# Performance work log

Hardware: AMD Instinct MI355X
Metric: run time of the kernel (lower is better)

Reference implementation:

```python
import jax, jax.numpy as jnp
import numpy as np
from jax import lax

EPS = 1e-5
PH = PW = 2  # patch size

def _bn(x, g, b, m, v):
    # eval-mode BatchNorm2d on NCHW
    scale = (g / jnp.sqrt(v + EPS))[None, :, None, None]
    return (x - m[None, :, None, None]) * scale + b[None, :, None, None]

def _gn1(x, g, b):
    # GroupNorm(num_groups=1): normalize over (C,P,N) per sample
    mu = x.mean(axis=(1, 2, 3), keepdims=True)
    var = x.var(axis=(1, 2, 3), keepdims=True)
    return (x - mu) / jnp.sqrt(var + EPS) * g[None, :, None, None] + b[None, :, None, None]

def _conv1x1(x, w, b=None):
    y = jnp.einsum('oc,bcpn->bopn', w, x)
    if b is not None:
        y = y + b[None, :, None, None]
    return y

def _silu(x):
    return x * jax.nn.sigmoid(x)

def _lin_attn(x, qkv_w, qkv_b, out_w, out_b, D):
    # x: [B, D, P, N]
    qkv = _conv1x1(x, qkv_w, qkv_b)            # [B, 2D+1, P, N]
    q = qkv[:, :1]                              # [B, 1, P, N]
    k = qkv[:, 1:1 + D]                         # [B, D, P, N]
    v = qkv[:, 1 + D:]                          # [B, D, P, N]
    scores = jax.nn.softmax(q, axis=-1)         # softmax over patches N
    ctx = jnp.sum(k * scores, axis=-1, keepdims=True)  # [B, D, P, 1]
    out = jax.nn.relu(v) * ctx
    return _conv1x1(out, out_w, out_b)

def reference(x, dw_w, dw_bn_g, dw_bn_b, dw_bn_m, dw_bn_v, pw_w,
              gn1_g, gn1_b, qkv_w, qkv_b, out_w, out_b,
              gn2_g, gn2_b, ffn1_w, ffn1_b, ffn2_w, ffn2_b,
              gnf_g, gnf_b, proj_w, proj_bn_g, proj_bn_b, proj_bn_m, proj_bn_v):
    B, C, H, W = x.shape
    D = pw_w.shape[0]
    L = gn1_g.shape[0]
    # local representation: depthwise 3x3 conv + BN + SiLU, then 1x1 to attn dim
    y = lax.conv_general_dilated(x, dw_w, (1, 1), 'SAME',
                                 feature_group_count=C,
                                 dimension_numbers=('NCHW', 'OIHW', 'NCHW'))
    y = _silu(_bn(y, dw_bn_g, dw_bn_b, dw_bn_m, dw_bn_v))
    y = _conv1x1(y, pw_w)                       # [B, D, H, W]
    # unfold to [B, D, P, N] (non-overlapping patches, torch F.unfold ordering)
    nH, nW = H // PH, W // PW
    p = y.reshape(B, D, nH, PH, nW, PW).transpose(0, 1, 3, 5, 2, 4).reshape(B, D, PH * PW, nH * nW)
    # global representation: L pre-norm linear-attention + FFN blocks
    for i in range(L):
        p = p + _lin_attn(_gn1(p, gn1_g[i], gn1_b[i]), qkv_w[i], qkv_b[i], out_w[i], out_b[i], D)
        h = _gn1(p, gn2_g[i], gn2_b[i])
        h = _silu(_conv1x1(h, ffn1_w[i], ffn1_b[i]))
        h = _conv1x1(h, ffn2_w[i], ffn2_b[i])
        p = p + h
    p = _gn1(p, gnf_g, gnf_b)
    # fold back to [B, D, H, W]
    y = p.reshape(B, D, PH, PW, nH, nW).transpose(0, 1, 4, 2, 5, 3).reshape(B, D, H, W)
    # projection back to in_channels: 1x1 conv + BN (no act)
    y = _conv1x1(y, proj_w)
    y = _bn(y, proj_bn_g, proj_bn_b, proj_bn_m, proj_bn_v)
    return y

def setup_inputs() -> dict:
    key = jax.random.key(0)
    ks = iter(jax.random.split(key, 40))
    def rn(shape, s=0.05):
        return jax.random.normal(next(ks), shape, jnp.float32) * s
    B, C, H, W, D, F, L = 16, 256, 64, 64, 256, 512, 2
    return dict(
        x=jax.random.normal(next(ks), (B, C, H, W), jnp.float32),
        dw_w=rn((C, 1, 3, 3), 0.2),
        dw_bn_g=jnp.ones((C,), jnp.float32), dw_bn_b=jnp.zeros((C,), jnp.float32),
        dw_bn_m=rn((C,), 0.01), dw_bn_v=jnp.ones((C,), jnp.float32),
        pw_w=rn((D, C)),
        gn1_g=jnp.ones((L, D), jnp.float32), gn1_b=jnp.zeros((L, D), jnp.float32),
        qkv_w=rn((L, 2 * D + 1, D)), qkv_b=jnp.zeros((L, 2 * D + 1), jnp.float32),
        out_w=rn((L, D, D)), out_b=jnp.zeros((L, D), jnp.float32),
        gn2_g=jnp.ones((L, D), jnp.float32), gn2_b=jnp.zeros((L, D), jnp.float32),
        ffn1_w=rn((L, F, D)), ffn1_b=jnp.zeros((L, F), jnp.float32),
        ffn2_w=rn((L, D, F)), ffn2_b=jnp.zeros((L, D), jnp.float32),
        gnf_g=jnp.ones((D,), jnp.float32), gnf_b=jnp.zeros((D,), jnp.float32),
        proj_w=rn((C, D)),
        proj_bn_g=jnp.ones((C,), jnp.float32), proj_bn_b=jnp.zeros((C,), jnp.float32),
        proj_bn_m=rn((C,), 0.01), proj_bn_v=jnp.ones((C,), jnp.float32),
    )
```

## Files before the change

### kernel.cpp

```cpp
#include <hip/hip_runtime.h>
#include <hip/hip_bf16.h>
#include <stdint.h>


#define B_    16
#define C_    256
#define D_    256
#define NPIX  4096
#define NE_PB 1048576

typedef __attribute__((ext_vector_type(8))) short  short8;
typedef __attribute__((ext_vector_type(4))) short  short4v;
typedef __attribute__((ext_vector_type(4))) float  f32x4;
typedef __attribute__((ext_vector_type(2))) float  f32x2;

__device__ __forceinline__ float b2f(short s){
  return __uint_as_float(((unsigned)(unsigned short)s) << 16);
}
__device__ __forceinline__ short f2b(float f){
  unsigned u = __float_as_uint(f);
  return (short)((u + 0x7fffu + ((u >> 16) & 1u)) >> 16);
}
__device__ __forceinline__ float silu_f(float x){ return x / (1.f + expf(-x)); }

__device__ __forceinline__ void gld16(const short* g, short* l){
  __builtin_amdgcn_global_load_lds(
      (const __attribute__((address_space(1))) void*)g,
      (__attribute__((address_space(3))) void*)l, 16, 0, 0);
}

__device__ __forceinline__ int pix2pi(int pix){
  int h = pix >> 6, w = pix & 63;
  return ((h & 1)*2 + (w & 1))*1024 + (h >> 1)*32 + (w >> 1);
}
__device__ __forceinline__ int pi2pix(int n){
  int p = n >> 10, idx = n & 1023;
  int h = ((idx >> 5) << 1) | (p >> 1);
  int w = ((idx & 31) << 1) | (p & 1);
  return h*64 + w;
}

__global__ void cvt6_k(const float* __restrict__ s0, const float* __restrict__ s1,
                       const float* __restrict__ s2, const float* __restrict__ s3,
                       const float* __restrict__ s4, const float* __restrict__ s5,
                       short* __restrict__ dst, float* __restrict__ stats){
  const int i = blockIdx.x*256 + threadIdx.x;
  if (blockIdx.x == 0 && threadIdx.x < 160) stats[threadIdx.x] = 0.f;
  if (i >= 1049088) return;
  float v;
  if      (i <  65536)  v = s0[i];
  else if (i < 328192)  v = s1[i -  65536];
  else if (i < 459264)  v = s2[i - 328192];
  else if (i < 721408)  v = s3[i - 459264];
  else if (i < 983552)  v = s4[i - 721408];
  else                  v = s5[i - 983552];
  dst[i] = f2b(v);
}

__global__ __launch_bounds__(256)
void dwconv_k(const float* __restrict__ X, const float* __restrict__ W,
              const float* __restrict__ G, const float* __restrict__ Bb,
              const float* __restrict__ Mn, const float* __restrict__ Vr,
              short* __restrict__ O){
  const int c = blockIdx.x, b = blockIdx.y;
  const int t = threadIdx.x;
  __shared__ float xs[66][68];
  if (t < 132){ int r = (t >= 66) ? 65 : 0; int cc = (t >= 66) ? t-66 : t; xs[r][cc] = 0.f; }
  if (t < 128){ int r = 1 + (t & 63); int cc = (t >> 6) ? 65 : 0; xs[r][cc] = 0.f; }
  const float* xp = X + ((size_t)(b*C_ + c)) * NPIX;
#pragma unroll
  for (int it = 0; it < 4; ++it){
    const int idx = it*256 + t;
    const int row = idx >> 4, cq = idx & 15;
    f32x4 v = *(const f32x4*)&xp[row*64 + cq*4];
    xs[row+1][cq*4+1] = v.x; xs[row+1][cq*4+2] = v.y;
    xs[row+1][cq*4+3] = v.z; xs[row+1][cq*4+4] = v.w;
  }
  float wgt[9];
#pragma unroll
  for (int j = 0; j < 9; ++j) wgt[j] = W[c*9 + j];
  const float scale = G[c] * rsqrtf(Vr[c] + 1e-5f);
  const float mu = Mn[c], bb = Bb[c];
  __syncthreads();
  const int tr = t >> 4, tc = t & 15;
  float win[6][6];
#pragma unroll
  for (int dr = 0; dr < 6; ++dr){
    f32x4 a = *(const f32x4*)&xs[tr*4+dr][tc*4];
    f32x2 bq = *(const f32x2*)&xs[tr*4+dr][tc*4+4];
    win[dr][0] = a.x; win[dr][1] = a.y; win[dr][2] = a.z; win[dr][3] = a.w;
    win[dr][4] = bq.x; win[dr][5] = bq.y;
  }
  short* op = O + ((size_t)(b*C_ + c)) * NPIX;
#pragma unroll
  for (int jr = 0; jr < 4; ++jr){
    short4v o;
#pragma unroll
    for (int jc = 0; jc < 4; ++jc){
      float s = 0.f;
#pragma unroll
      for (int dh = 0; dh < 3; ++dh)
#pragma unroll
        for (int dw = 0; dw < 3; ++dw)
          s += win[jr+dh][jc+dw] * wgt[dh*3+dw];
      float y = (s - mu) * scale + bb;
      o[jc] = f2b(silu_f(y));
    }
    *(short4v*)&op[(tr*4+jr)*64 + tc*4] = o;
  }
}

__global__ void transpose_k(const short* __restrict__ I, short* __restrict__ O){
  const int s0 = blockIdx.x*64, c0 = blockIdx.y*64, b = blockIdx.z;
  const int t = threadIdx.x;
  __shared__ short tile[64][68];
  const int hi = t >> 4, lo = t & 15;
#pragma unroll
  for (int cy = 0; cy < 4; ++cy){
    const int cl = cy*16 + hi;
    short4v v = *(const short4v*)&I[((size_t)(b*C_ + c0 + cl))*NPIX + s0 + lo*4];
    tile[lo*4+0][cl] = v.x; tile[lo*4+1][cl] = v.y;
    tile[lo*4+2][cl] = v.z; tile[lo*4+3][cl] = v.w;
  }
  __syncthreads();
#pragma unroll
  for (int py = 0; py < 4; ++py){
    const int pl = py*16 + hi;
    short4v v = *(const short4v*)&tile[pl][lo*4];
    *(short4v*)&O[((size_t)(b*NPIX + s0 + pl))*C_ + c0 + lo*4] = v;
  }
}

template<int EPI, int K>
__global__ __launch_bounds__(256, 3)
void gemm_k(const short* __restrict__ Wt, const short* __restrict__ X,
            const int M,
            const float* __restrict__ bias,
            short* __restrict__ P,
            short* __restrict__ Obf,
            float* __restrict__ Of32,
            const float* __restrict__ bng, const float* __restrict__ bnb,
            const float* __restrict__ bnm, const float* __restrict__ bnv,
            float* __restrict__ st)
{
  constexpr int S = K / 64;
  const int nt = blockIdx.x;
  const int ct = blockIdx.y;
  const int b  = blockIdx.z;
  const int tid = threadIdx.x;
  const int ln = tid & 63, wv = tid >> 6;
  const int wx = wv & 1;
  const int wy = wv >> 1;
  const int lr = ln & 15, lq = ln >> 4;
  const int rl = ln >> 3, sp = ln & 7;
  const int sw = sp ^ rl;

  __shared__ __align__(16) char smem[33824];
  short* As = (short*)smem;
  short* Xs = (short*)(smem + 16384);
  float* CT = (float*)smem;
  float* red = (float*)(smem + 33792);

  const short* Wp = Wt + (size_t)(ct*128)*K;
  const short* Xp = X + ((size_t)b*NPIX + (size_t)nt*128) * K;

  const short* gw[4]; const short* gx[4]; short* lw[4]; short* lx[4];
#pragma unroll
  for (int j = 0; j < 4; ++j){
    const int row = 32*wv + 8*j + rl;
    gw[j] = Wp + (size_t)row*K + sw*8;
    gx[j] = Xp + (size_t)row*K + sw*8;
    lw[j] = As + (4*wv + j)*512;
    lx[j] = Xs + (4*wv + j)*512;
  }

  f32x4 acc[4][4];
#pragma unroll
  for (int r = 0; r < 4; ++r)
#pragma unroll
    for (int c = 0; c < 4; ++c) acc[r][c] = (f32x4){0.f,0.f,0.f,0.f};

  for (int stp = 0; stp < S; ++stp){
    if (stp) __syncthreads();
#pragma unroll
    for (int j = 0; j < 4; ++j) gld16(gw[j] + stp*64, lw[j]);
#pragma unroll
    for (int j = 0; j < 4; ++j) gld16(gx[j] + stp*64, lx[j]);
    __syncthreads();
#pragma unroll
    for (int kk = 0; kk < 2; ++kk){
      const int seg = ((kk*4 + lq) ^ (lr & 7)) * 16;
      short8 aw[4], bx[4];
#pragma unroll
      for (int r = 0; r < 4; ++r)
        aw[r] = *(const short8*)((const char*)As + (wx*64 + r*16 + lr)*128 + seg);
#pragma unroll
      for (int c = 0; c < 4; ++c)
        bx[c] = *(const short8*)((const char*)Xs + (wy*64 + c*16 + lr)*128 + seg);
#pragma unroll
      for (int r = 0; r < 4; ++r)
#pragma unroll
        for (int c = 0; c < 4; ++c)
          acc[r][c] = __builtin_amdgcn_mfma_f32_16x16x32_bf16(aw[r], bx[c], acc[r][c], 0, 0, 0);
    }
  }

  const int ch8 = (tid & 15) * 8;
  f32x4 bv0 = (f32x4){0.f,0.f,0.f,0.f}, bv1 = bv0;
  if constexpr (EPI == 1 || EPI == 2 || EPI == 3 || EPI == 5){
    bv0 = *(const f32x4*)&bias[ct*128 + ch8];
    bv1 = *(const f32x4*)&bias[ct*128 + ch8 + 4];
  }

  float sm = 0.f, ss = 0.f;

  if constexpr (EPI != 4){
#pragma unroll
    for (int p = 0; p < 2; ++p){
      __syncthreads();
      if (wy == p){
#pragma unroll
        for (int r = 0; r < 4; ++r)
#pragma unroll
          for (int c = 0; c < 4; ++c)
            *(f32x4*)&CT[(c*16 + lr)*132 + wx*64 + r*16 + lq*4] = acc[r][c];
      }
      __syncthreads();
#pragma unroll
      for (int it = 0; it < 4; ++it){
        const int pixL = it*16 + (tid >> 4);
        f32x4 v0 = *(const f32x4*)&CT[pixL*132 + ch8];
        f32x4 v1 = *(const f32x4*)&CT[pixL*132 + ch8 + 4];
        v0.x += bv0.x; v0.y += bv0.y; v0.z += bv0.z; v0.w += bv0.w;
        v1.x += bv1.x; v1.y += bv1.y; v1.z += bv1.z; v1.w += bv1.w;
        int pixg = nt*128 + p*64 + pixL;
        if constexpr (EPI == 5) pixg = pi2pix(pixg);
        const size_t rowb = (size_t)b*NPIX + pixg;
        if constexpr (EPI == 0){
          short8 o;
          o[0]=f2b(v0.x); o[1]=f2b(v0.y); o[2]=f2b(v0.z); o[3]=f2b(v0.w);
          o[4]=f2b(v1.x); o[5]=f2b(v1.y); o[6]=f2b(v1.z); o[7]=f2b(v1.w);
          *(short8*)&P[rowb*256 + ct*128 + ch8] = o;
          sm += v0.x+v0.y+v0.z+v0.w + v1.x+v1.y+v1.z+v1.w;
          ss += v0.x*v0.x+v0.y*v0.y+v0.z*v0.z+v0.w*v0.w
              + v1.x*v1.x+v1.y*v1.y+v1.z*v1.z+v1.w*v1.w;
        } else if constexpr (EPI == 2 || EPI == 5){
          short* pp = &P[rowb*256 + ct*128 + ch8];
          short8 old = *(const short8*)pp;
          float n0 = b2f(old[0])+v0.x, n1 = b2f(old[1])+v0.y;
          float n2 = b2f(old[2])+v0.z, n3 = b2f(old[3])+v0.w;
          float n4 = b2f(old[4])+v1.x, n5 = b2f(old[5])+v1.y;
          float n6 = b2f(old[6])+v1.z, n7 = b2f(old[7])+v1.w;
          short8 o;
          o[0]=f2b(n0); o[1]=f2b(n1); o[2]=f2b(n2); o[3]=f2b(n3);
          o[4]=f2b(n4); o[5]=f2b(n5); o[6]=f2b(n6); o[7]=f2b(n7);
          *(short8*)pp = o;
          sm += n0+n1+n2+n3+n4+n5+n6+n7;
          ss += n0*n0+n1*n1+n2*n2+n3*n3+n4*n4+n5*n5+n6*n6+n7*n7;
        } else if constexpr (EPI == 1){
          short8 o;
          o[0]=f2b(v0.x); o[1]=f2b(v0.y); o[2]=f2b(v0.z); o[3]=f2b(v0.w);
          o[4]=f2b(v1.x); o[5]=f2b(v1.y); o[6]=f2b(v1.z); o[7]=f2b(v1.w);
          *(short8*)&Obf[rowb*(size_t)M + ct*128 + ch8] = o;
        } else {
          short8 o;
          o[0]=f2b(silu_f(v0.x)); o[1]=f2b(silu_f(v0.y));
          o[2]=f2b(silu_f(v0.z)); o[3]=f2b(silu_f(v0.w));
          o[4]=f2b(silu_f(v1.x)); o[5]=f2b(silu_f(v1.y));
          o[6]=f2b(silu_f(v1.z)); o[7]=f2b(silu_f(v1.w));
          *(short8*)&Obf[rowb*(size_t)M + ct*128 + ch8] = o;
        }
      }
    }
    if constexpr (EPI == 0 || EPI == 2 || EPI == 5){
#pragma unroll
      for (int o = 32; o > 0; o >>= 1){ sm += __shfl_down(sm, o); ss += __shfl_down(ss, o); }
      if (ln == 0){ red[wv*2] = sm; red[wv*2+1] = ss; }
      __syncthreads();
      if (tid == 0){
        atomicAdd(&st[b*2+0], red[0]+red[2]+red[4]+red[6]);
        atomicAdd(&st[b*2+1], red[1]+red[3]+red[5]+red[7]);
      }
    }
  } else {
#pragma unroll
    for (int p = 0; p < 2; ++p){
      __syncthreads();
      if (wx == p){
#pragma unroll
        for (int r = 0; r < 4; ++r)
#pragma unroll
          for (int c = 0; c < 4; ++c){
            const int pixL = wy*64 + c*16 + lr;
#pragma unroll
            for (int j = 0; j < 4; ++j)
              CT[(r*16 + lq*4 + j)*132 + pixL] = acc[r][c][j];
          }
      }
      __syncthreads();
#pragma unroll
      for (int it = 0; it < 8; ++it){
        const int idx = it*256 + tid;
        const int chL = idx >> 5, pq = (idx & 31)*4;
        const int chan = ct*128 + p*64 + chL;
        f32x4 v = *(const f32x4*)&CT[chL*132 + pq];
        const float sc = bng[chan] * rsqrtf(bnv[chan] + 1e-5f);
        const float mu = bnm[chan], bb = bnb[chan];
        f32x4 o;
        o.x = (v.x - mu)*sc + bb; o.y = (v.y - mu)*sc + bb;
        o.z = (v.z - mu)*sc + bb; o.w = (v.w - mu)*sc + bb;
        *(f32x4*)&Of32[((size_t)(b*C_ + chan))*NPIX + (size_t)nt*128 + pq] = o;
      }
    }
  }
}

template<bool PERM>
__global__ void gn_apply_k(const short* __restrict__ P, const float* __restrict__ st,
                           const float* __restrict__ G, const float* __restrict__ Bb,
                           short* __restrict__ U){
  const int b = blockIdx.y;
  const float mean = st[b*2]   * (1.f/NE_PB);
  const float var  = st[b*2+1] * (1.f/NE_PB) - mean*mean;
  const float inv  = rsqrtf(var + 1e-5f);
  const int t = threadIdx.x;
  const int c0 = (t*8) & 255;
  const f32x4 g0 = *(const f32x4*)&G[c0],  g1 = *(const f32x4*)&G[c0+4];
  const f32x4 b0 = *(const f32x4*)&Bb[c0], b1 = *(const f32x4*)&Bb[c0+4];
#pragma unroll
  for (int i = 0; i < 16; ++i){
    const int e = blockIdx.x*32768 + t*8 + i*2048;
    short8 pv = *(const short8*)&P[(size_t)b*NE_PB + e];
    short8 o;
    o[0] = f2b((b2f(pv[0]) - mean)*inv*g0.x + b0.x);
    o[1] = f2b((b2f(pv[1]) - mean)*inv*g0.y + b0.y);
    o[2] = f2b((b2f(pv[2]) - mean)*inv*g0.z + b0.z);
    o[3] = f2b((b2f(pv[3]) - mean)*inv*g0.w + b0.w);
    o[4] = f2b((b2f(pv[4]) - mean)*inv*g1.x + b1.x);
    o[5] = f2b((b2f(pv[5]) - mean)*inv*g1.y + b1.y);
    o[6] = f2b((b2f(pv[6]) - mean)*inv*g1.z + b1.z);
    o[7] = f2b((b2f(pv[7]) - mean)*inv*g1.w + b1.w);
    if constexpr (PERM){
      const int pix = e >> 8;
      *(short8*)&U[((size_t)b*NPIX + pix2pi(pix))*256 + c0] = o;
    } else {
      *(short8*)&U[(size_t)b*NE_PB + e] = o;
    }
  }
}

__global__ void q_k(const short* __restrict__ U, const float* __restrict__ Wq,
                    const float* __restrict__ Qb, float* __restrict__ Q){
  const int lane = threadIdx.x & 63;
  const int pix = (blockIdx.x*256 + threadIdx.x) >> 6;
  short4v u4 = *(const short4v*)&U[(size_t)pix*256 + lane*4];
  f32x4  w4 = *(const f32x4*)&Wq[lane*4];
  float s = b2f(u4.x)*w4.x + b2f(u4.y)*w4.y + b2f(u4.z)*w4.z + b2f(u4.w)*w4.w;
#pragma unroll
  for (int o = 32; o > 0; o >>= 1) s += __shfl_down(s, o);
  if (lane == 0) Q[pix] = s + Qb[0];
}

__global__ void softmax_k(const float* __restrict__ Q, float* __restrict__ S,
                          float* __restrict__ CT){
  const int bp = blockIdx.x;
  const int t = threadIdx.x;
  CT[bp*256 + t] = 0.f;
  float vals[4];
  float mx = -1e30f;
#pragma unroll
  for (int j = 0; j < 4; ++j){
    vals[j] = Q[bp*1024 + t + j*256];
    mx = fmaxf(mx, vals[j]);
  }
  __shared__ float red[4];
  const int lane = t & 63, wv = t >> 6;
#pragma unroll
  for (int o = 32; o > 0; o >>= 1) mx = fmaxf(mx, __shfl_down(mx, o));
  if (lane == 0) red[wv] = mx;
  __syncthreads();
  mx = fmaxf(fmaxf(red[0], red[1]), fmaxf(red[2], red[3]));
  __syncthreads();
  float sum = 0.f;
#pragma unroll
  for (int j = 0; j < 4; ++j){ vals[j] = expf(vals[j] - mx); sum += vals[j]; }
#pragma unroll
  for (int o = 32; o > 0; o >>= 1) sum += __shfl_down(sum, o);
  if (lane == 0) red[wv] = sum;
  __syncthreads();
  sum = red[0] + red[1] + red[2] + red[3];
  const float r = 1.f / sum;
#pragma unroll
  for (int j = 0; j < 4; ++j) S[bp*1024 + t + j*256] = vals[j]*r;
}

__global__ void ctx_k(const short* __restrict__ KV, const float* __restrict__ S,
                      float* __restrict__ CT){
  const int bp = blockIdx.x, ch = blockIdx.y;
  const int ln = threadIdx.x & 63, wv = threadIdx.x >> 6;
  const int j0 = ch*256 + wv*64;
  f32x4 acc = (f32x4){0.f,0.f,0.f,0.f};
  for (int jj = 0; jj < 64; jj += 4){
    f32x4 s4 = *(const f32x4*)&S[bp*1024 + j0 + jj];
#pragma unroll
    for (int u = 0; u < 4; ++u){
      short4v kv = *(const short4v*)&KV[((size_t)bp*1024 + j0 + jj + u)*512 + ln*4];
      const float s = s4[u];
      acc.x += b2f(kv.x)*s; acc.y += b2f(kv.y)*s;
      acc.z += b2f(kv.z)*s; acc.w += b2f(kv.w)*s;
    }
  }
  atomicAdd(&CT[bp*256 + ln*4 + 0], acc.x);
  atomicAdd(&CT[bp*256 + ln*4 + 1], acc.y);
  atomicAdd(&CT[bp*256 + ln*4 + 2], acc.z);
  atomicAdd(&CT[bp*256 + ln*4 + 3], acc.w);
}

__global__ void attn_in_k(const short* __restrict__ KV, const float* __restrict__ CT,
                          short* __restrict__ O){
  const size_t vid = (size_t)blockIdx.x*256 + threadIdx.x;
  const int c4 = (int)(vid & 63);
  const size_t r = vid >> 6;
  const int bp = (int)(r >> 10);
  short4v v4 = *(const short4v*)&KV[r*512 + 256 + c4*4];
  f32x4  cx = *(const f32x4*)&CT[bp*256 + c4*4];
  short4v o;
  o.x = f2b(fmaxf(b2f(v4.x), 0.f)*cx.x);
  o.y = f2b(fmaxf(b2f(v4.y), 0.f)*cx.y);
  o.z = f2b(fmaxf(b2f(v4.z), 0.f)*cx.z);
  o.w = f2b(fmaxf(b2f(v4.w), 0.f)*cx.w);
  *(short4v*)&O[r*256 + c4*4] = o;
}

extern "C" void kernel_launch(void* const* d_in, const int* in_sizes, int n_in,
                              void* d_out, int out_size, void* d_ws, size_t ws_size,
                              hipStream_t stream){
  const float* x      = (const float*)d_in[0];
  const float* dw_w   = (const float*)d_in[1];
  const float* dw_g   = (const float*)d_in[2];
  const float* dw_b   = (const float*)d_in[3];
  const float* dw_m   = (const float*)d_in[4];
  const float* dw_v   = (const float*)d_in[5];
  const float* pw_w   = (const float*)d_in[6];
  const float* gn1_g  = (const float*)d_in[7];
  const float* gn1_b  = (const float*)d_in[8];
  const float* qkv_w  = (const float*)d_in[9];
  const float* qkv_b  = (const float*)d_in[10];
  const float* out_w  = (const float*)d_in[11];
  const float* out_b  = (const float*)d_in[12];
  const float* gn2_g  = (const float*)d_in[13];
  const float* gn2_b  = (const float*)d_in[14];
  const float* ffn1_w = (const float*)d_in[15];
  const float* ffn1_b = (const float*)d_in[16];
  const float* ffn2_w = (const float*)d_in[17];
  const float* ffn2_b = (const float*)d_in[18];
  const float* gnf_g  = (const float*)d_in[19];
  const float* gnf_b  = (const float*)d_in[20];
  const float* proj_w = (const float*)d_in[21];
  const float* pbn_g  = (const float*)d_in[22];
  const float* pbn_b  = (const float*)d_in[23];
  const float* pbn_m  = (const float*)d_in[24];
  const float* pbn_v  = (const float*)d_in[25];
  float* out = (float*)d_out;

  uint8_t* w8 = (uint8_t*)d_ws;
  short* P     = (short*)(w8);
  short* bufA  = (short*)(w8 + 33554432);
  short* bufB  = (short*)(w8 + 67108864);
  short* wbase = (short*)(w8 + 134217728);
  short* w_pw  = wbase;
  short* w_qkv = wbase + 65536;
  short* w_out = wbase + 328192;
  short* w_f1  = wbase + 459264;
  short* w_f2  = wbase + 721408;
  short* w_pj  = wbase + 983552;
  float* qbuf  = (float*)(w8 + 136315904);
  float* scor  = (float*)(w8 + 136578048);
  float* ctxs  = (float*)(w8 + 136840192);
  float* stats = (float*)(w8 + 136905728);

  cvt6_k<<<4098, 256, 0, stream>>>(pw_w, qkv_w, out_w, ffn1_w, ffn2_w, proj_w,
                                   wbase, stats);

  dwconv_k<<<dim3(256,16), 256, 0, stream>>>(x, dw_w, dw_g, dw_b, dw_m, dw_v, bufB);
  transpose_k<<<dim3(64,4,16), 256, 0, stream>>>(bufB, bufA);

  gemm_k<0,256><<<dim3(32,2,16), 256, 0, stream>>>(w_pw, bufA, 256, nullptr, P,
      nullptr, nullptr, nullptr, nullptr, nullptr, nullptr, stats + 0);

  for (int i = 0; i < 2; ++i){
    float* st1 = stats + (i == 0 ? 0 : 2*32);
    gn_apply_k<true><<<dim3(32,16), 256, 0, stream>>>(P, st1, gn1_g + i*256, gn1_b + i*256, bufA);
    q_k<<<16384, 256, 0, stream>>>(bufA, qkv_w + i*513*256, qkv_b + i*513, qbuf);
    gemm_k<1,256><<<dim3(32,4,16), 256, 0, stream>>>(w_qkv + (i*513+1)*256, bufA, 512,
        qkv_b + i*513 + 1, nullptr, bufB, nullptr, nullptr, nullptr, nullptr, nullptr, nullptr);
    softmax_k<<<64, 256, 0, stream>>>(qbuf, scor, ctxs);
    ctx_k<<<dim3(64,4), 256, 0, stream>>>(bufB, scor, ctxs);
    attn_in_k<<<16384, 256, 0, stream>>>(bufB, ctxs, bufA);
    gemm_k<5,256><<<dim3(32,2,16), 256, 0, stream>>>(w_out + i*65536, bufA, 256,
        out_b + i*256, P, nullptr, nullptr, nullptr, nullptr, nullptr, nullptr,
        stats + (i == 0 ? 1 : 3)*32);
    float* st2 = stats + (i == 0 ? 1 : 3)*32;
    gn_apply_k<false><<<dim3(32,16), 256, 0, stream>>>(P, st2, gn2_g + i*256, gn2_b + i*256, bufA);
    gemm_k<3,256><<<dim3(32,4,16), 256, 0, stream>>>(w_f1 + i*131072, bufA, 512,
        ffn1_b + i*512, nullptr, bufB, nullptr, nullptr, nullptr, nullptr, nullptr, nullptr);
    gemm_k<2,512><<<dim3(32,2,16), 256, 0, stream>>>(w_f2 + i*131072, bufB, 256,
        ffn2_b + i*256, P, nullptr, nullptr, nullptr, nullptr, nullptr, nullptr,
        stats + (i == 0 ? 2 : 4)*32);
  }

  gn_apply_k<false><<<dim3(32,16), 256, 0, stream>>>(P, stats + 4*32, gnf_g, gnf_b, bufA);
  gemm_k<4,256><<<dim3(32,2,16), 256, 0, stream>>>(w_pj, bufA, 256, nullptr,
      nullptr, nullptr, out, pbn_g, pbn_b, pbn_m, pbn_v, nullptr);

  (void)in_sizes; (void)n_in; (void)out_size; (void)ws_size;
}
```

Baseline: 636.6 us.

## Fold GroupNorm into downstream GEMM weights and epilogues, drop gn_apply passes

Folds the GroupNorm gamma into the converted bf16 weights and precomputes per-output-row sums of W·gamma and W·beta, so each GEMM epilogue applies the per-sample mean and inverse std as a scale-and-bias. This removes all five gn_apply kernels, each of which read and wrote the full activation tensor. The patch permutation is moved into the qkv GEMM's load addressing and into q_k's gather. The cost is that the normalization now runs on unnormalized bf16 activations, which changes rounding, and the qkv GEMM loads gathered rows with less contiguous addressing.

```diff
diff --git a/kernel.cpp b/kernel.cpp
--- a/kernel.cpp
+++ b/kernel.cpp
@@ -29,10 +29,6 @@
       (__attribute__((address_space(3))) void*)l, 16, 0, 0);
 }
 
-__device__ __forceinline__ int pix2pi(int pix){
-  int h = pix >> 6, w = pix & 63;
-  return ((h & 1)*2 + (w & 1))*1024 + (h >> 1)*32 + (w >> 1);
-}
 __device__ __forceinline__ int pi2pix(int n){
   int p = n >> 10, idx = n & 1023;
   int h = ((idx >> 5) << 1) | (p >> 1);
@@ -43,18 +39,49 @@
 __global__ void cvt6_k(const float* __restrict__ s0, const float* __restrict__ s1,
                        const float* __restrict__ s2, const float* __restrict__ s3,
                        const float* __restrict__ s4, const float* __restrict__ s5,
+                       const float* __restrict__ g1, const float* __restrict__ g2,
+                       const float* __restrict__ gf,
                        short* __restrict__ dst, float* __restrict__ stats){
   const int i = blockIdx.x*256 + threadIdx.x;
   if (blockIdx.x == 0 && threadIdx.x < 160) stats[threadIdx.x] = 0.f;
   if (i >= 1049088) return;
   float v;
-  if      (i <  65536)  v = s0[i];
-  else if (i < 328192)  v = s1[i -  65536];
-  else if (i < 459264)  v = s2[i - 328192];
-  else if (i < 721408)  v = s3[i - 459264];
-  else if (i < 983552)  v = s4[i - 721408];
-  else                  v = s5[i - 983552];
+  if      (i <  65536){ v = s0[i]; }
+  else if (i < 328192){ int j = i -  65536;
+                        v = s1[j] * g1[(j/131328)*256 + (j & 255)]; }
+  else if (i < 459264){ v = s2[i - 328192]; }
+  else if (i < 721408){ int j = i - 459264;
+                        v = s3[j] * g2[(j >> 17)*256 + (j & 255)]; }
+  else if (i < 983552){ v = s4[i - 721408]; }
+  else               { int j = i - 983552;
+                        v = s5[j] * gf[j & 255]; }
   dst[i] = f2b(v);
+}
+
+__global__ void fold_k(const float* __restrict__ qkvw, const float* __restrict__ f1w,
+                       const float* __restrict__ pjw,
+                       const float* __restrict__ g1, const float* __restrict__ b1,
+                       const float* __restrict__ g2, const float* __restrict__ b2,
+                       const float* __restrict__ gf, const float* __restrict__ bf,
+                       float* __restrict__ uv){
+  const int row = blockIdx.x;
+  const int l = threadIdx.x;
+  const float* W; const float* g; const float* bb;
+  if (row < 1026){ int layer = row/513, o = row - layer*513;
+    W = qkvw + (size_t)(layer*513 + o)*256; g = g1 + layer*256; bb = b1 + layer*256; }
+  else if (row < 2050){ int r2 = row - 1026; int layer = r2 >> 9, o = r2 & 511;
+    W = f1w + (size_t)(layer*512 + o)*256; g = g2 + layer*256; bb = b2 + layer*256; }
+  else { int o = row - 2050; W = pjw + (size_t)o*256; g = gf; bb = bf; }
+  float u = 0.f, v = 0.f;
+#pragma unroll
+  for (int k = 0; k < 4; ++k){
+    const int c = l + k*64;
+    const float w = W[c];
+    u += w * g[c]; v += w * bb[c];
+  }
+#pragma unroll
+  for (int o = 32; o > 0; o >>= 1){ u += __shfl_down(u, o); v += __shfl_down(v, o); }
+  if (l == 0){ uv[row*2] = u; uv[row*2+1] = v; }
 }
 
 __global__ __launch_bounds__(256)
@@ -131,7 +158,7 @@
   }
 }
 
-template<int EPI, int K>
+template<int EPI, int K, int FOLD, int GATHER>
 __global__ __launch_bounds__(256, 3)
 void gemm_k(const short* __restrict__ Wt, const short* __restrict__ X,
             const int M,
@@ -141,7 +168,8 @@
             float* __restrict__ Of32,
             const float* __restrict__ bng, const float* __restrict__ bnb,
             const float* __restrict__ bnm, const float* __restrict__ bnv,
-            float* __restrict__ st)
+            float* __restrict__ st,
+            const float* __restrict__ uv, const float* __restrict__ stIn)
 {
   constexpr int S = K / 64;
   const int nt = blockIdx.x;
@@ -169,7 +197,10 @@
   for (int j = 0; j < 4; ++j){
     const int row = 32*wv + 8*j + rl;
     gw[j] = Wp + (size_t)row*K + sw*8;
-    gx[j] = Xp + (size_t)row*K + sw*8;
+    if constexpr (GATHER)
+      gx[j] = X + ((size_t)b*NPIX + pi2pix(nt*128 + row))*K + sw*8;
+    else
+      gx[j] = Xp + (size_t)row*K + sw*8;
     lw[j] = As + (4*wv + j)*512;
     lx[j] = Xs + (4*wv + j)*512;
   }
@@ -206,10 +237,26 @@
   }
 
   const int ch8 = (tid & 15) * 8;
-  f32x4 bv0 = (f32x4){0.f,0.f,0.f,0.f}, bv1 = bv0;
+  float s_mul = 1.f;
+  f32x4 be0 = (f32x4){0.f,0.f,0.f,0.f}, be1 = be0;
   if constexpr (EPI == 1 || EPI == 2 || EPI == 3 || EPI == 5){
-    bv0 = *(const f32x4*)&bias[ct*128 + ch8];
-    bv1 = *(const f32x4*)&bias[ct*128 + ch8 + 4];
+    be0 = *(const f32x4*)&bias[ct*128 + ch8];
+    be1 = *(const f32x4*)&bias[ct*128 + ch8 + 4];
+  }
+  if constexpr (FOLD && EPI != 4){
+    const float mean = stIn[b*2]   * (1.f/NE_PB);
+    const float m2   = stIn[b*2+1] * (1.f/NE_PB);
+    const float inv  = rsqrtf(m2 - mean*mean + 1e-5f);
+    s_mul = inv;
+    const float muinv = mean * inv;
+    const float* up = &uv[(size_t)(ct*128 + ch8)*2];
+#pragma unroll
+    for (int k = 0; k < 4; ++k){
+      f32x2 p0 = *(const f32x2*)&up[k*2];
+      f32x2 p1 = *(const f32x2*)&up[8 + k*2];
+      be0[k] += p0.y - muinv*p0.x;
+      be1[k] += p1.y - muinv*p1.x;
+    }
   }
 
   float sm = 0.f, ss = 0.f;
@@ -231,8 +278,12 @@
         const int pixL = it*16 + (tid >> 4);
         f32x4 v0 = *(const f32x4*)&CT[pixL*132 + ch8];
         f32x4 v1 = *(const f32x4*)&CT[pixL*132 + ch8 + 4];
-        v0.x += bv0.x; v0.y += bv0.y; v0.z += bv0.z; v0.w += bv0.w;
-        v1.x += bv1.x; v1.y += bv1.y; v1.z += bv1.z; v1.w += bv1.w;
+        if constexpr (EPI != 0){
+          v0.x = v0.x*s_mul + be0.x; v0.y = v0.y*s_mul + be0.y;
+          v0.z = v0.z*s_mul + be0.z; v0.w = v0.w*s_mul + be0.w;
+          v1.x = v1.x*s_mul + be1.x; v1.y = v1.y*s_mul + be1.y;
+          v1.z = v1.z*s_mul + be1.z; v1.w = v1.w*s_mul + be1.w;
+        }
         int pixg = nt*128 + p*64 + pixL;
         if constexpr (EPI == 5) pixg = pi2pix(pixg);
         const size_t rowb = (size_t)b*NPIX + pixg;
@@ -283,6 +334,14 @@
       }
     }
   } else {
+    float muinv4 = 0.f;
+    if constexpr (FOLD){
+      const float mean = stIn[b*2]   * (1.f/NE_PB);
+      const float m2   = stIn[b*2+1] * (1.f/NE_PB);
+      const float inv  = rsqrtf(m2 - mean*mean + 1e-5f);
+      s_mul = inv;
+      muinv4 = mean * inv;
+    }
 #pragma unroll
     for (int p = 0; p < 2; ++p){
       __syncthreads();
@@ -306,59 +365,42 @@
         f32x4 v = *(const f32x4*)&CT[chL*132 + pq];
         const float sc = bng[chan] * rsqrtf(bnv[chan] + 1e-5f);
         const float mu = bnm[chan], bb = bnb[chan];
+        float A = sc, Bc = -mu*sc + bb;
+        if constexpr (FOLD){
+          f32x2 uvp = *(const f32x2*)&uv[(size_t)chan*2];
+          A = s_mul * sc;
+          Bc = ((uvp.y - muinv4*uvp.x) - mu)*sc + bb;
+        }
         f32x4 o;
-        o.x = (v.x - mu)*sc + bb; o.y = (v.y - mu)*sc + bb;
-        o.z = (v.z - mu)*sc + bb; o.w = (v.w - mu)*sc + bb;
+        o.x = v.x*A + Bc; o.y = v.y*A + Bc;
+        o.z = v.z*A + Bc; o.w = v.w*A + Bc;
         *(f32x4*)&Of32[((size_t)(b*C_ + chan))*NPIX + (size_t)nt*128 + pq] = o;
       }
     }
   }
 }
 
-template<bool PERM>
-__global__ void gn_apply_k(const short* __restrict__ P, const float* __restrict__ st,
-                           const float* __restrict__ G, const float* __restrict__ Bb,
-                           short* __restrict__ U){
-  const int b = blockIdx.y;
-  const float mean = st[b*2]   * (1.f/NE_PB);
-  const float var  = st[b*2+1] * (1.f/NE_PB) - mean*mean;
-  const float inv  = rsqrtf(var + 1e-5f);
-  const int t = threadIdx.x;
-  const int c0 = (t*8) & 255;
-  const f32x4 g0 = *(const f32x4*)&G[c0],  g1 = *(const f32x4*)&G[c0+4];
-  const f32x4 b0 = *(const f32x4*)&Bb[c0], b1 = *(const f32x4*)&Bb[c0+4];
-#pragma unroll
-  for (int i = 0; i < 16; ++i){
-    const int e = blockIdx.x*32768 + t*8 + i*2048;
-    short8 pv = *(const short8*)&P[(size_t)b*NE_PB + e];
-    short8 o;
-    o[0] = f2b((b2f(pv[0]) - mean)*inv*g0.x + b0.x);
-    o[1] = f2b((b2f(pv[1]) - mean)*inv*g0.y + b0.y);
-    o[2] = f2b((b2f(pv[2]) - mean)*inv*g0.z + b0.z);
-    o[3] = f2b((b2f(pv[3]) - mean)*inv*g0.w + b0.w);
-    o[4] = f2b((b2f(pv[4]) - mean)*inv*g1.x + b1.x);
-    o[5] = f2b((b2f(pv[5]) - mean)*inv*g1.y + b1.y);
-    o[6] = f2b((b2f(pv[6]) - mean)*inv*g1.z + b1.z);
-    o[7] = f2b((b2f(pv[7]) - mean)*inv*g1.w + b1.w);
-    if constexpr (PERM){
-      const int pix = e >> 8;
-      *(short8*)&U[((size_t)b*NPIX + pix2pi(pix))*256 + c0] = o;
-    } else {
-      *(short8*)&U[(size_t)b*NE_PB + e] = o;
-    }
-  }
-}
-
-__global__ void q_k(const short* __restrict__ U, const float* __restrict__ Wq,
-                    const float* __restrict__ Qb, float* __restrict__ Q){
+__global__ void q_k(const short* __restrict__ P, const float* __restrict__ Wq,
+                    const float* __restrict__ Gg, const float* __restrict__ Qb,
+                    const float* __restrict__ uv, const float* __restrict__ stIn,
+                    float* __restrict__ Q){
   const int lane = threadIdx.x & 63;
   const int pix = (blockIdx.x*256 + threadIdx.x) >> 6;
-  short4v u4 = *(const short4v*)&U[(size_t)pix*256 + lane*4];
+  const int b = pix >> 12, pi = pix & 4095;
+  const int prow = pi2pix(pi);
+  short4v u4 = *(const short4v*)&P[((size_t)b*NPIX + prow)*256 + lane*4];
   f32x4  w4 = *(const f32x4*)&Wq[lane*4];
-  float s = b2f(u4.x)*w4.x + b2f(u4.y)*w4.y + b2f(u4.z)*w4.z + b2f(u4.w)*w4.w;
+  f32x4  g4 = *(const f32x4*)&Gg[lane*4];
+  float s = b2f(u4.x)*w4.x*g4.x + b2f(u4.y)*w4.y*g4.y
+          + b2f(u4.z)*w4.z*g4.z + b2f(u4.w)*w4.w*g4.w;
 #pragma unroll
   for (int o = 32; o > 0; o >>= 1) s += __shfl_down(s, o);
-  if (lane == 0) Q[pix] = s + Qb[0];
+  if (lane == 0){
+    const float mean = stIn[b*2]   * (1.f/NE_PB);
+    const float m2   = stIn[b*2+1] * (1.f/NE_PB);
+    const float inv  = rsqrtf(m2 - mean*mean + 1e-5f);
+    Q[pix] = inv*s + Qb[0] + uv[1] - inv*mean*uv[0];
+  }
 }
 
 __global__ void softmax_k(const float* __restrict__ Q, float* __restrict__ S,
@@ -478,40 +520,45 @@
   float* scor  = (float*)(w8 + 136578048);
   float* ctxs  = (float*)(w8 + 136840192);
   float* stats = (float*)(w8 + 136905728);
+  float* uvb   = (float*)(w8 + 136906368);
 
   cvt6_k<<<4098, 256, 0, stream>>>(pw_w, qkv_w, out_w, ffn1_w, ffn2_w, proj_w,
-                                   wbase, stats);
+                                   gn1_g, gn2_g, gnf_g, wbase, stats);
+  fold_k<<<2306, 64, 0, stream>>>(qkv_w, ffn1_w, proj_w,
+                                  gn1_g, gn1_b, gn2_g, gn2_b, gnf_g, gnf_b, uvb);
 
   dwconv_k<<<dim3(256,16), 256, 0, stream>>>(x, dw_w, dw_g, dw_b, dw_m, dw_v, bufB);
   transpose_k<<<dim3(64,4,16), 256, 0, stream>>>(bufB, bufA);
 
-  gemm_k<0,256><<<dim3(32,2,16), 256, 0, stream>>>(w_pw, bufA, 256, nullptr, P,
-      nullptr, nullptr, nullptr, nullptr, nullptr, nullptr, stats + 0);
+  gemm_k<0,256,0,0><<<dim3(32,2,16), 256, 0, stream>>>(w_pw, bufA, 256, nullptr, P,
+      nullptr, nullptr, nullptr, nullptr, nullptr, nullptr, stats + 0,
+      nullptr, nullptr);
 
   for (int i = 0; i < 2; ++i){
-    float* st1 = stats + (i == 0 ? 0 : 2*32);
-    gn_apply_k<true><<<dim3(32,16), 256, 0, stream>>>(P, st1, gn1_g + i*256, gn1_b + i*256, bufA);
-    q_k<<<16384, 256, 0, stream>>>(bufA, qkv_w + i*513*256, qkv_b + i*513, qbuf);
-    gemm_k<1,256><<<dim3(32,4,16), 256, 0, stream>>>(w_qkv + (i*513+1)*256, bufA, 512,
-        qkv_b + i*513 + 1, nullptr, bufB, nullptr, nullptr, nullptr, nullptr, nullptr, nullptr);
+    float* st1 = stats + (i == 0 ? 0 : 2)*32;
+    q_k<<<16384, 256, 0, stream>>>(P, qkv_w + (size_t)i*513*256, gn1_g + i*256,
+        qkv_b + i*513, uvb + (size_t)(i*513)*2, st1, qbuf);
+    gemm_k<1,256,1,1><<<dim3(32,4,16), 256, 0, stream>>>(w_qkv + (i*513+1)*256, P, 512,
+        qkv_b + i*513 + 1, nullptr, bufB, nullptr, nullptr, nullptr, nullptr, nullptr,
+        nullptr, uvb + (size_t)(i*513+1)*2, st1);
     softmax_k<<<64, 256, 0, stream>>>(qbuf, scor, ctxs);
     ctx_k<<<dim3(64,4), 256, 0, stream>>>(bufB, scor, ctxs);
     attn_in_k<<<16384, 256, 0, stream>>>(bufB, ctxs, bufA);
-    gemm_k<5,256><<<dim3(32,2,16), 256, 0, stream>>>(w_out + i*65536, bufA, 256,
+    gemm_k<5,256,0,0><<<dim3(32,2,16), 256, 0, stream>>>(w_out + i*65536, bufA, 256,
         out_b + i*256, P, nullptr, nullptr, nullptr, nullptr, nullptr, nullptr,
-        stats + (i == 0 ? 1 : 3)*32);
+        stats + (i == 0 ? 1 : 3)*32, nullptr, nullptr);
     float* st2 = stats + (i == 0 ? 1 : 3)*32;
-    gn_apply_k<false><<<dim3(32,16), 256, 0, stream>>>(P, st2, gn2_g + i*256, gn2_b + i*256, bufA);
-    gemm_k<3,256><<<dim3(32,4,16), 256, 0, stream>>>(w_f1 + i*131072, bufA, 512,
-        ffn1_b + i*512, nullptr, bufB, nullptr, nullptr, nullptr, nullptr, nullptr, nullptr);
-    gemm_k<2,512><<<dim3(32,2,16), 256, 0, stream>>>(w_f2 + i*131072, bufB, 256,
+    gemm_k<3,256,1,0><<<dim3(32,4,16), 256, 0, stream>>>(w_f1 + i*131072, P, 512,
+        ffn1_b + i*512, nullptr, bufB, nullptr, nullptr, nullptr, nullptr, nullptr,
+        nullptr, uvb + (size_t)(1026 + i*512)*2, st2);
+    gemm_k<2,512,0,0><<<dim3(32,2,16), 256, 0, stream>>>(w_f2 + i*131072, bufB, 256,
         ffn2_b + i*256, P, nullptr, nullptr, nullptr, nullptr, nullptr, nullptr,
-        stats + (i == 0 ? 2 : 4)*32);
-  }
-
-  gn_apply_k<false><<<dim3(32,16), 256, 0, stream>>>(P, stats + 4*32, gnf_g, gnf_b, bufA);
-  gemm_k<4,256><<<dim3(32,2,16), 256, 0, stream>>>(w_pj, bufA, 256, nullptr,
-      nullptr, nullptr, out, pbn_g, pbn_b, pbn_m, pbn_v, nullptr);
+        stats + (i == 0 ? 2 : 4)*32, nullptr, nullptr);
+  }
+
+  gemm_k<4,256,1,0><<<dim3(32,2,16), 256, 0, stream>>>(w_pj, P, 256, nullptr,
+      nullptr, nullptr, out, pbn_g, pbn_b, pbn_m, pbn_v, nullptr,
+      uvb + (size_t)2050*2, stats + 4*32);
 
   (void)in_sizes; (void)n_in; (void)out_size; (void)ws_size;
 }
```

Measured after the change: 623.8 us. 2.0% less time.
